# Kernel tuning notes

Hardware: AMD Instinct MI355X
Metric: run time of the kernel (lower is better)

Reference implementation:

```python
import jax, jax.numpy as jnp
import numpy as np

N, D = 16384, 256

def setup_inputs() -> dict:
    key = jax.random.key(0)
    k1, k2 = jax.random.split(key)
    z_a = jax.random.normal(k1, (N, D), dtype=jnp.float32)
    z_b = jax.random.normal(k2, (N, D), dtype=jnp.float32)
    bias = jnp.zeros((), dtype=jnp.float32)  # learnable bias, init 0
    return {"z_a": z_a, "z_b": z_b, "bias": bias}

def reference(z_a, z_b, bias):
    # sim[i,j] = z_a[i] . z_b[j]
    sim = jnp.einsum("nd,md->nm", z_a, z_b)  # [N, N]
    n = sim.shape[0]
    # targets: +1 on diagonal, -1 off-diagonal
    targets = 2.0 * jnp.eye(n, dtype=sim.dtype) - 1.0
    logits = targets * sim + bias
    # mean(-log_sigmoid(logits))
    return -jnp.mean(jax.nn.log_sigmoid(logits))
```

## Files before the change

kernel.cpp:

```cpp
#include <hip/hip_runtime.h>
#include <hip/hip_bf16.h>

#define Nn 16384
#define Dd 256
#define L2E 1.4426950408889634f
#define LN2 0.6931471805599453f

typedef __attribute__((ext_vector_type(8))) int int8v;
typedef __attribute__((ext_vector_type(16))) float f32x16;
typedef __attribute__((ext_vector_type(2))) float f32x2;

__device__ inline void gload_lds16(const void* g, void* l) {
    __builtin_amdgcn_global_load_lds(
        (const __attribute__((address_space(1))) void*)g,
        (__attribute__((address_space(3))) void*)l, 16, 0, 0);
}

__global__ __launch_bounds__(256) void cvt_kernel(
        const float4* __restrict__ a, const float4* __restrict__ b,
        int2* __restrict__ oa, int2* __restrict__ ob) {
    int i = blockIdx.x * 256 + threadIdx.x;
    float4 a0 = a[2 * i], a1 = a[2 * i + 1];
    float4 b0 = b[2 * i], b1 = b[2 * i + 1];
    int alo = __builtin_amdgcn_cvt_pk_fp8_f32(a0.x * L2E, a0.y * L2E, 0, false);
    alo     = __builtin_amdgcn_cvt_pk_fp8_f32(a0.z * L2E, a0.w * L2E, alo, true);
    int ahi = __builtin_amdgcn_cvt_pk_fp8_f32(a1.x * L2E, a1.y * L2E, 0, false);
    ahi     = __builtin_amdgcn_cvt_pk_fp8_f32(a1.z * L2E, a1.w * L2E, ahi, true);
    int blo = __builtin_amdgcn_cvt_pk_fp8_f32(b0.x, b0.y, 0, false);
    blo     = __builtin_amdgcn_cvt_pk_fp8_f32(b0.z, b0.w, blo, true);
    int bhi = __builtin_amdgcn_cvt_pk_fp8_f32(b1.x, b1.y, 0, false);
    bhi     = __builtin_amdgcn_cvt_pk_fp8_f32(b1.z, b1.w, bhi, true);
    oa[i] = make_int2(alo, ahi);
    ob[i] = make_int2(blo, bhi);
}

__device__ inline int8v rdoff(const unsigned char* base, int olo, int ohi) {
    int4 lo = *(const int4*)&base[olo];
    int4 hi = *(const int4*)&base[ohi];
    int8v r;
    r[0] = lo.x; r[1] = lo.y; r[2] = lo.z; r[3] = lo.w;
    r[4] = hi.x; r[5] = hi.y; r[6] = hi.z; r[7] = hi.w;
    return r;
}

#define MFMA_(A, B, C) __builtin_amdgcn_mfma_scale_f32_32x32x64_f8f6f4(       \
    (A), (B), (C), 0, 0, 0, 0x7F7F7F7F, 0, 0x7F7F7F7F)

__global__ __launch_bounds__(256, 2) void siglip_kernel(
        const unsigned char* __restrict__ ga,
        const unsigned char* __restrict__ gb,
        const float* __restrict__ bp,
        float* __restrict__ out) {
    __shared__ unsigned char As[128 * 256];
    __shared__ unsigned char Bs0[64 * 256];
    __shared__ unsigned char Bs1[64 * 256];
    __shared__ float wsum[4];

    const int tid  = threadIdx.x;
    const int lane = tid & 63;
    const int wid  = tid >> 6;
    const int wm   = wid >> 1;
    const int wn   = wid & 1;
    const int l31  = lane & 31;
    const int h    = lane >> 5;

    const int bid = blockIdx.x;
    const int nid = (bid & 7) * 256 + (bid >> 3);
    const int by  = nid >> 4;
    const int bxs = nid & 15;
    const size_t rowA0 = (size_t)by * 128;
    const int    rB0   = bxs * 1024;

    const float b2 = bp[0] * L2E;
    const int diagblk = (bxs == (by >> 3));
    const int dby7    = by & 7;

#pragma unroll
    for (int p = 0; p < 8; ++p) {
        int c = p * 256 + tid; int row = c >> 4;
        int scl = (c & 15) ^ (row & 15);
        gload_lds16(&ga[(rowA0 + row) * Dd + scl * 16], &As[c * 16]);
    }

    const unsigned char* gp[4];
#pragma unroll
    for (int p = 0; p < 4; ++p) {
        int c = p * 256 + tid; int row = c >> 4;
        int scl = (c & 15) ^ (row & 15);
        gp[p] = &gb[(size_t)(rB0 + row) * 256 + scl * 16];
    }
#define STAGE_ADV(BBUF)                                                       \
    {                                                                         \
        _Pragma("unroll")                                                     \
        for (int p = 0; p < 4; ++p) {                                         \
            gload_lds16(gp[p], &(BBUF)[(p * 256 + tid) * 16]);                \
            gp[p] += 16384;                                                   \
        }                                                                     \
    }
    STAGE_ADV(Bs0)
    STAGE_ADV(Bs1)

    int offA[16], offB[8];
#pragma unroll
    for (int s = 0; s < 4; ++s) {
        int cb = s * 4 + h * 2;
#pragma unroll
        for (int mf = 0; mf < 2; ++mf) {
            int rr = wm * 64 + mf * 32 + l31;
            int x  = rr & 15;
            offA[s * 4 + mf * 2 + 0] = rr * 256 + ((cb) ^ x) * 16;
            offA[s * 4 + mf * 2 + 1] = rr * 256 + ((cb + 1) ^ x) * 16;
        }
        int rb = wn * 32 + l31;
        int xb = rb & 15;
        offB[s * 2 + 0] = rb * 256 + ((cb) ^ xb) * 16;
        offB[s * 2 + 1] = rb * 256 + ((cb + 1) ^ xb) * 16;
    }

    f32x16 bias_acc;
#pragma unroll
    for (int q = 0; q < 16; ++q) bias_acc[q] = -b2;

    asm volatile("s_waitcnt vmcnt(4)" ::: "memory");
    __builtin_amdgcn_s_barrier();
    asm volatile("" ::: "memory");

    f32x2 sm = {0.f, 0.f}, se = {0.f, 0.f};
    float ld = 0.f;

#define PANEL(BBUF, T, DO_STAGE)                                              \
    {                                                                         \
        f32x16 acc[2];                                                        \
        {                                                                     \
            int8v aF0 = rdoff(As, offA[0], offA[1]);                          \
            int8v aF1 = rdoff(As, offA[2], offA[3]);                          \
            int8v bF  = rdoff(BBUF, offB[0], offB[1]);                        \
            acc[0] = MFMA_(aF0, bF, bias_acc);                                \
            acc[1] = MFMA_(aF1, bF, bias_acc);                                \
        }                                                                     \
        _Pragma("unroll")                                                     \
        for (int s = 1; s < 4; ++s) {                                         \
            int8v aF0 = rdoff(As, offA[s * 4 + 0], offA[s * 4 + 1]);          \
            int8v aF1 = rdoff(As, offA[s * 4 + 2], offA[s * 4 + 3]);          \
            int8v bF  = rdoff(BBUF, offB[s * 2 + 0], offB[s * 2 + 1]);        \
            acc[0] = MFMA_(aF0, bF, acc[0]);                                  \
            acc[1] = MFMA_(aF1, bF, acc[1]);                                  \
        }                                                                     \
        asm volatile("" ::: "memory");                                        \
        __builtin_amdgcn_s_barrier();                                         \
        asm volatile("" ::: "memory");                                        \
        if (DO_STAGE) STAGE_ADV(BBUF)                                         \
        _Pragma("unroll")                                                     \
        for (int mf = 0; mf < 2; ++mf)                                        \
            _Pragma("unroll")                                                 \
            for (int q = 0; q < 16; q += 2) {                                 \
                f32x2 yv = {acc[mf][q], acc[mf][q + 1]};                      \
                f32x2 mv = {fmaxf(yv[0], 0.f), fmaxf(yv[1], 0.f)};            \
                sm += mv;                                                     \
                f32x2 ev = {__builtin_amdgcn_exp2f(-fabsf(yv[0])),            \
                            __builtin_amdgcn_exp2f(-fabsf(yv[1]))};           \
                se += ev;                                                     \
            }                                                                 \
        if (diagblk && ((T) >> 1) == dby7 && wm == ((T) & 1)) {               \
            const int mfd = wn;                                               \
            _Pragma("unroll")                                                 \
            for (int q = 0; q < 16; ++q) {                                    \
                int rq = (q & 3) + 8 * (q >> 2) + 4 * h;                      \
                if (rq == l31) {                                              \
                    float y  = acc[mfd][q];                                   \
                    float u  = -(y + 2.f * b2);                               \
                    float ey = __builtin_amdgcn_exp2f(-fabsf(y));             \
                    float eu = __builtin_amdgcn_exp2f(-fabsf(u));             \
                    ld += (LN2 * fmaxf(u, 0.f) + eu) -                        \
                          (LN2 * fmaxf(y, 0.f) + ey);                         \
                }                                                             \
            }                                                                 \
        }                                                                     \
    }

#define WAIT4  asm volatile("s_waitcnt vmcnt(4)" ::: "memory");               \
               __builtin_amdgcn_s_barrier(); asm volatile("" ::: "memory");
#define WAIT0  asm volatile("s_waitcnt vmcnt(0)" ::: "memory");               \
               __builtin_amdgcn_s_barrier(); asm volatile("" ::: "memory");

#pragma unroll 1
    for (int tt = 0; tt < 7; ++tt) {
        PANEL(Bs0, tt * 2, 1)
        WAIT4
        PANEL(Bs1, tt * 2 + 1, 1)
        WAIT4
    }
    PANEL(Bs0, 14, 0)
    WAIT0
    PANEL(Bs1, 15, 0)

    float v = fmaf(LN2, sm[0] + sm[1], se[0] + se[1] + ld);

#pragma unroll
    for (int off = 32; off; off >>= 1)
        v += __shfl_down(v, off);
    if (lane == 0) wsum[wid] = v;
    __syncthreads();
    if (tid == 0) {
        float t = wsum[0] + wsum[1] + wsum[2] + wsum[3];
        atomicAdd(out, t * (1.0f / ((float)Nn * (float)Nn)));
    }
#undef STAGE_ADV
#undef PANEL
#undef WAIT4
#undef WAIT0
}

extern "C" void kernel_launch(void* const* d_in, const int* in_sizes, int n_in,
                              void* d_out, int out_size, void* d_ws, size_t ws_size,
                              hipStream_t stream) {
    const float* za   = (const float*)d_in[0];
    const float* zb   = (const float*)d_in[1];
    const float* bias = (const float*)d_in[2];

    unsigned char* wa = (unsigned char*)d_ws;
    unsigned char* wb = wa + (size_t)Nn * Dd;

    hipMemsetAsync(d_out, 0, sizeof(float), stream);

    cvt_kernel<<<dim3(Nn * Dd / 2048), 256, 0, stream>>>(
        (const float4*)za, (const float4*)zb, (int2*)wa, (int2*)wb);

    siglip_kernel<<<dim3(2048), 256, 0, stream>>>(wa, wb, bias, (float*)d_out);
}
```

Before: 116.6 us.

## Enlarge block to 16 waves with 128-row B panels and one tile per wave

Switches the similarity kernel from 4-wave blocks over 64-row B panels to 1024-thread blocks over 128-row B panels, giving each wave a single 32x32 output tile. The panel loop is fully unrolled over 8 panels and staging, wait counts and the final reduction are adjusted to match. The aim is more waves per CU to hide load and exp latency and fewer panel iterations. In exchange each wave loses A-fragment reuse across two MFMAs, LDS use per block grows to about 96KB, and barriers must synchronise 16 waves.

```diff
diff --git a/kernel.cpp b/kernel.cpp
--- a/kernel.cpp
+++ b/kernel.cpp
@@ -46,21 +46,21 @@
 #define MFMA_(A, B, C) __builtin_amdgcn_mfma_scale_f32_32x32x64_f8f6f4(       \
     (A), (B), (C), 0, 0, 0, 0x7F7F7F7F, 0, 0x7F7F7F7F)
 
-__global__ __launch_bounds__(256, 2) void siglip_kernel(
+__global__ __launch_bounds__(1024, 4) void siglip_kernel(
         const unsigned char* __restrict__ ga,
         const unsigned char* __restrict__ gb,
         const float* __restrict__ bp,
         float* __restrict__ out) {
     __shared__ unsigned char As[128 * 256];
-    __shared__ unsigned char Bs0[64 * 256];
-    __shared__ unsigned char Bs1[64 * 256];
-    __shared__ float wsum[4];
+    __shared__ unsigned char Bs0[128 * 256];
+    __shared__ unsigned char Bs1[128 * 256];
+    __shared__ float wsum[16];
 
     const int tid  = threadIdx.x;
     const int lane = tid & 63;
     const int wid  = tid >> 6;
-    const int wm   = wid >> 1;
-    const int wn   = wid & 1;
+    const int wm   = wid >> 2;
+    const int wn   = wid & 3;
     const int l31  = lane & 31;
     const int h    = lane >> 5;
 
@@ -73,55 +73,52 @@
 
     const float b2 = bp[0] * L2E;
     const int diagblk = (bxs == (by >> 3));
-    const int dby7    = by & 7;
-
-#pragma unroll
-    for (int p = 0; p < 8; ++p) {
-        int c = p * 256 + tid; int row = c >> 4;
+    const int dpan    = by & 7;
+
+#pragma unroll
+    for (int p = 0; p < 2; ++p) {
+        int c = p * 1024 + tid; int row = c >> 4;
         int scl = (c & 15) ^ (row & 15);
         gload_lds16(&ga[(rowA0 + row) * Dd + scl * 16], &As[c * 16]);
     }
 
-    const unsigned char* gp[4];
-#pragma unroll
-    for (int p = 0; p < 4; ++p) {
-        int c = p * 256 + tid; int row = c >> 4;
+    const unsigned char* gp[2];
+#pragma unroll
+    for (int p = 0; p < 2; ++p) {
+        int c = p * 1024 + tid; int row = c >> 4;
         int scl = (c & 15) ^ (row & 15);
         gp[p] = &gb[(size_t)(rB0 + row) * 256 + scl * 16];
     }
 #define STAGE_ADV(BBUF)                                                       \
     {                                                                         \
         _Pragma("unroll")                                                     \
-        for (int p = 0; p < 4; ++p) {                                         \
-            gload_lds16(gp[p], &(BBUF)[(p * 256 + tid) * 16]);                \
-            gp[p] += 16384;                                                   \
+        for (int p = 0; p < 2; ++p) {                                         \
+            gload_lds16(gp[p], &(BBUF)[(p * 1024 + tid) * 16]);               \
+            gp[p] += 32768;                                                   \
         }                                                                     \
     }
     STAGE_ADV(Bs0)
     STAGE_ADV(Bs1)
 
-    int offA[16], offB[8];
-#pragma unroll
-    for (int s = 0; s < 4; ++s) {
-        int cb = s * 4 + h * 2;
-#pragma unroll
-        for (int mf = 0; mf < 2; ++mf) {
-            int rr = wm * 64 + mf * 32 + l31;
-            int x  = rr & 15;
-            offA[s * 4 + mf * 2 + 0] = rr * 256 + ((cb) ^ x) * 16;
-            offA[s * 4 + mf * 2 + 1] = rr * 256 + ((cb + 1) ^ x) * 16;
+    int offA[8], offB[8];
+    {
+        int ra = wm * 32 + l31, xa = ra & 15;
+        int rb = wn * 32 + l31, xb = rb & 15;
+#pragma unroll
+        for (int s = 0; s < 4; ++s) {
+            int cb = s * 4 + h * 2;
+            offA[s * 2 + 0] = ra * 256 + ((cb) ^ xa) * 16;
+            offA[s * 2 + 1] = ra * 256 + ((cb + 1) ^ xa) * 16;
+            offB[s * 2 + 0] = rb * 256 + ((cb) ^ xb) * 16;
+            offB[s * 2 + 1] = rb * 256 + ((cb + 1) ^ xb) * 16;
         }
-        int rb = wn * 32 + l31;
-        int xb = rb & 15;
-        offB[s * 2 + 0] = rb * 256 + ((cb) ^ xb) * 16;
-        offB[s * 2 + 1] = rb * 256 + ((cb + 1) ^ xb) * 16;
     }
 
     f32x16 bias_acc;
 #pragma unroll
     for (int q = 0; q < 16; ++q) bias_acc[q] = -b2;
 
-    asm volatile("s_waitcnt vmcnt(4)" ::: "memory");
+    asm volatile("s_waitcnt vmcnt(2)" ::: "memory");
     __builtin_amdgcn_s_barrier();
     asm volatile("" ::: "memory");
 
@@ -130,44 +127,37 @@
 
 #define PANEL(BBUF, T, DO_STAGE)                                              \
     {                                                                         \
-        f32x16 acc[2];                                                        \
+        f32x16 acc;                                                           \
         {                                                                     \
-            int8v aF0 = rdoff(As, offA[0], offA[1]);                          \
-            int8v aF1 = rdoff(As, offA[2], offA[3]);                          \
-            int8v bF  = rdoff(BBUF, offB[0], offB[1]);                        \
-            acc[0] = MFMA_(aF0, bF, bias_acc);                                \
-            acc[1] = MFMA_(aF1, bF, bias_acc);                                \
+            int8v aF = rdoff(As, offA[0], offA[1]);                           \
+            int8v bF = rdoff(BBUF, offB[0], offB[1]);                         \
+            acc = MFMA_(aF, bF, bias_acc);                                    \
         }                                                                     \
         _Pragma("unroll")                                                     \
         for (int s = 1; s < 4; ++s) {                                         \
-            int8v aF0 = rdoff(As, offA[s * 4 + 0], offA[s * 4 + 1]);          \
-            int8v aF1 = rdoff(As, offA[s * 4 + 2], offA[s * 4 + 3]);          \
-            int8v bF  = rdoff(BBUF, offB[s * 2 + 0], offB[s * 2 + 1]);        \
-            acc[0] = MFMA_(aF0, bF, acc[0]);                                  \
-            acc[1] = MFMA_(aF1, bF, acc[1]);                                  \
+            int8v aF = rdoff(As, offA[s * 2 + 0], offA[s * 2 + 1]);           \
+            int8v bF = rdoff(BBUF, offB[s * 2 + 0], offB[s * 2 + 1]);         \
+            acc = MFMA_(aF, bF, acc);                                         \
         }                                                                     \
         asm volatile("" ::: "memory");                                        \
         __builtin_amdgcn_s_barrier();                                         \
         asm volatile("" ::: "memory");                                        \
         if (DO_STAGE) STAGE_ADV(BBUF)                                         \
         _Pragma("unroll")                                                     \
-        for (int mf = 0; mf < 2; ++mf)                                        \
-            _Pragma("unroll")                                                 \
-            for (int q = 0; q < 16; q += 2) {                                 \
-                f32x2 yv = {acc[mf][q], acc[mf][q + 1]};                      \
-                f32x2 mv = {fmaxf(yv[0], 0.f), fmaxf(yv[1], 0.f)};            \
-                sm += mv;                                                     \
-                f32x2 ev = {__builtin_amdgcn_exp2f(-fabsf(yv[0])),            \
-                            __builtin_amdgcn_exp2f(-fabsf(yv[1]))};           \
-                se += ev;                                                     \
-            }                                                                 \
-        if (diagblk && ((T) >> 1) == dby7 && wm == ((T) & 1)) {               \
-            const int mfd = wn;                                               \
+        for (int q = 0; q < 16; q += 2) {                                     \
+            f32x2 yv = {acc[q], acc[q + 1]};                                  \
+            f32x2 mv = {fmaxf(yv[0], 0.f), fmaxf(yv[1], 0.f)};                \
+            sm += mv;                                                         \
+            f32x2 ev = {__builtin_amdgcn_exp2f(-fabsf(yv[0])),                \
+                        __builtin_amdgcn_exp2f(-fabsf(yv[1]))};               \
+            se += ev;                                                         \
+        }                                                                     \
+        if (diagblk && (T) == dpan && wm == wn) {                             \
             _Pragma("unroll")                                                 \
             for (int q = 0; q < 16; ++q) {                                    \
                 int rq = (q & 3) + 8 * (q >> 2) + 4 * h;                      \
                 if (rq == l31) {                                              \
-                    float y  = acc[mfd][q];                                   \
+                    float y  = acc[q];                                        \
                     float u  = -(y + 2.f * b2);                               \
                     float ey = __builtin_amdgcn_exp2f(-fabsf(y));             \
                     float eu = __builtin_amdgcn_exp2f(-fabsf(u));             \
@@ -178,21 +168,19 @@
         }                                                                     \
     }
 
-#define WAIT4  asm volatile("s_waitcnt vmcnt(4)" ::: "memory");               \
+#define WAIT2  asm volatile("s_waitcnt vmcnt(2)" ::: "memory");               \
                __builtin_amdgcn_s_barrier(); asm volatile("" ::: "memory");
 #define WAIT0  asm volatile("s_waitcnt vmcnt(0)" ::: "memory");               \
                __builtin_amdgcn_s_barrier(); asm volatile("" ::: "memory");
 
-#pragma unroll 1
-    for (int tt = 0; tt < 7; ++tt) {
-        PANEL(Bs0, tt * 2, 1)
-        WAIT4
-        PANEL(Bs1, tt * 2 + 1, 1)
-        WAIT4
-    }
-    PANEL(Bs0, 14, 0)
-    WAIT0
-    PANEL(Bs1, 15, 0)
+    PANEL(Bs0, 0, 1)  WAIT2
+    PANEL(Bs1, 1, 1)  WAIT2
+    PANEL(Bs0, 2, 1)  WAIT2
+    PANEL(Bs1, 3, 1)  WAIT2
+    PANEL(Bs0, 4, 1)  WAIT2
+    PANEL(Bs1, 5, 1)  WAIT2
+    PANEL(Bs0, 6, 0)  WAIT0
+    PANEL(Bs1, 7, 0)
 
     float v = fmaf(LN2, sm[0] + sm[1], se[0] + se[1] + ld);
 
@@ -202,12 +190,14 @@
     if (lane == 0) wsum[wid] = v;
     __syncthreads();
     if (tid == 0) {
-        float t = wsum[0] + wsum[1] + wsum[2] + wsum[3];
+        float t = 0.f;
+#pragma unroll
+        for (int w = 0; w < 16; ++w) t += wsum[w];
         atomicAdd(out, t * (1.0f / ((float)Nn * (float)Nn)));
     }
 #undef STAGE_ADV
 #undef PANEL
-#undef WAIT4
+#undef WAIT2
 #undef WAIT0
 }
 
@@ -226,5 +216,5 @@
     cvt_kernel<<<dim3(Nn * Dd / 2048), 256, 0, stream>>>(
         (const float4*)za, (const float4*)zb, (int2*)wa, (int2*)wb);
 
-    siglip_kernel<<<dim3(2048), 256, 0, stream>>>(wa, wb, bias, (float*)d_out);
-}
+    siglip_kernel<<<dim3(2048), 1024, 0, stream>>>(wa, wb, bias, (float*)d_out);
+}
```

Result: slower. 463.0 us (+297.0%).
